# Optimization experiments

Measured on AMD Instinct MI355X. Metric: run time of the kernel, lower is better.

The kernel has to match this reference:

```python
import jax, jax.numpy as jnp
import numpy as np

N_NODES = 100000
N_EDGES = 300000
N_TYPES = 3
HID = 128
EMB = 64
N_GRAPHS = 4096
T_STEPS = 4


def setup_inputs() -> dict:
    key = jax.random.key(0)
    ks = jax.random.split(key, 12)
    s = 1.0 / np.sqrt(HID)
    return {
        "node_features": jax.random.normal(ks[0], (N_NODES, HID), jnp.float32),
        "edge_index": jax.random.randint(ks[1], (N_TYPES, 2, N_EDGES), 0, N_NODES),
        "node_to_graph_id": jnp.sort(jax.random.randint(ks[2], (N_NODES,), 0, N_GRAPHS)),
        "W_msg": jax.random.normal(ks[3], (N_TYPES, HID, HID), jnp.float32) * s,
        "b_msg": jnp.zeros((N_TYPES, HID), jnp.float32),
        "W_ih": jax.random.normal(ks[4], (3 * HID, HID), jnp.float32) * s,
        "W_hh": jax.random.normal(ks[5], (3 * HID, HID), jnp.float32) * s,
        "b_ih": jnp.zeros((3 * HID,), jnp.float32),
        "b_hh": jnp.zeros((3 * HID,), jnp.float32),
        "W_proj": jax.random.normal(ks[6], (EMB, HID), jnp.float32) * s,
        "b_proj": jnp.zeros((EMB,), jnp.float32),
        "W_gate": jax.random.normal(ks[7], (EMB, HID), jnp.float32) * s,
        "b_gate": jnp.zeros((EMB,), jnp.float32),
    }


def _gru_cell(m, h, W_ih, W_hh, b_ih, b_hh):
    # torch.nn.GRUCell math; gates ordered (r, z, n)
    gi = m @ W_ih.T + b_ih          # [N, 3H]
    gh = h @ W_hh.T + b_hh          # [N, 3H]
    i_r, i_z, i_n = jnp.split(gi, 3, axis=-1)
    h_r, h_z, h_n = jnp.split(gh, 3, axis=-1)
    r = jax.nn.sigmoid(i_r + h_r)
    z = jax.nn.sigmoid(i_z + h_z)
    n = jnp.tanh(i_n + r * h_n)
    return (1.0 - z) * n + z * h


def reference(node_features, edge_index, node_to_graph_id,
              W_msg, b_msg, W_ih, W_hh, b_ih, b_hh,
              W_proj, b_proj, W_gate, b_gate):
    h = node_features  # [N, H]

    def per_type(eidx, W, b, h):
        src, dst = eidx[0], eidx[1]
        m = h[src] @ W + b  # gather + per-edge-type linear, [E, H]
        return jax.ops.segment_sum(m, dst, num_segments=N_NODES)

    for _ in range(T_STEPS):  # fixed small T: python loop is fine
        msgs = jax.vmap(per_type, in_axes=(0, 0, 0, None))(edge_index, W_msg, b_msg, h)
        m = msgs.sum(axis=0)  # [N, H] aggregated over edge types
        h = _gru_cell(m, h, W_ih, W_hh, b_ih, b_hh)

    # gated index_add graph readout (mlp_down is identity)
    proj = h @ W_proj.T + b_proj                 # [N, E]
    gate = jax.nn.sigmoid(h @ W_gate.T + b_gate)  # [N, E]
    graph_feats = jax.ops.segment_sum(gate * proj, node_to_graph_id,
                                      num_segments=N_GRAPHS)
    return graph_feats
```

## Files before the change

kernel.cpp:

```cpp
#include <hip/hip_runtime.h>
#include <hip/hip_bf16.h>
#include <math.h>

#define NN 100000
#define NNP 100096
#define NE 300000
#define HID 128
#define EMB 64
#define NG 4096
#define DEG_CAP 32
#define XS 512

typedef __bf16 bf16x8 __attribute__((ext_vector_type(8)));
typedef float  f32x16 __attribute__((ext_vector_type(16)));
typedef short  short8 __attribute__((ext_vector_type(8)));

typedef const __attribute__((address_space(1))) unsigned int* gas_u32;
typedef __attribute__((address_space(3))) unsigned int* las_u32;

__device__ __forceinline__ void gload16(const void* g, void* l) {
    __builtin_amdgcn_global_load_lds((gas_u32)g, (las_u32)l, 16, 0, 0);
}
__device__ __forceinline__ void gload16nt(const void* g, void* l) {
    __builtin_amdgcn_global_load_lds((gas_u32)g, (las_u32)l, 16, 0, 2);
}

__device__ __forceinline__ float bf2f(unsigned short u) {
    unsigned int x = ((unsigned int)u) << 16;
    return __builtin_bit_cast(float, x);
}
__device__ __forceinline__ unsigned short f2bf(float f) {
    unsigned int x = __builtin_bit_cast(unsigned int, f);
    unsigned int r = x + 0x7fff + ((x >> 16) & 1);
    return (unsigned short)(r >> 16);
}
__device__ __forceinline__ float sigm(float x) { return 1.f / (1.f + __expf(-x)); }

__global__ __launch_bounds__(256) void k_init(const float* __restrict__ nf,
                                              unsigned short* __restrict__ Y) {
    int id = blockIdx.x * 256 + threadIdx.x;
    int n = id >> 7, c = id & 127;
    Y[(long)n * HID + c] = (n < NN) ? f2bf(nf[(long)n * HID + c]) : (unsigned short)0;
}

__global__ __launch_bounds__(256) void k_build_csr(const int* __restrict__ ei,
                                                   int* __restrict__ deg,
                                                   int* __restrict__ csr) {
    int id = blockIdx.x * 256 + threadIdx.x;
    if (id >= 3 * NE) return;
    int t = id / NE;
    int i = id - t * NE;
    int src = ei[(t * 2 + 0) * NE + i];
    int dst = ei[(t * 2 + 1) * NE + i];
    int p = atomicAdd(&deg[t * NN + dst], 1);
    if (p < DEG_CAP) csr[((long)t * NN + dst) * DEG_CAP + p] = src;
}

__global__ __launch_bounds__(256) void k_pack_deg(const int* __restrict__ deg,
                                                  int4* __restrict__ degp) {
    int n = blockIdx.x * 256 + threadIdx.x;
    if (n >= NNP) return;
    int4 v; v.x = 0; v.y = 0; v.z = 0; v.w = 0;
    if (n < NN) { v.x = deg[n]; v.y = deg[NN + n]; v.z = deg[2 * NN + n]; }
    degp[n] = v;
}

__global__ __launch_bounds__(512) void k_build_w(const float* __restrict__ Wmsg,
                                                 const float* __restrict__ Wih,
                                                 const float* __restrict__ Whh,
                                                 unsigned short* __restrict__ Bf) {
    int np = blockIdx.x;
    int k = threadIdx.x;
    int c = np >> 2, sec = np & 3;
    float v = 0.f;
    if (k < 384) {
        if (sec < 3) {
            int t = k >> 7, kk = k & 127;
            const float* wm = Wmsg + ((long)t * HID + kk) * HID;
            const float* wi = Wih + (long)(sec * HID + c) * HID;
            float s = 0.f;
            for (int j = 0; j < HID; j++) s += wm[j] * wi[j];
            v = s;
        }
    } else {
        int kk = k - 384;
        if (sec == 0)      v = Whh[(long)c * HID + kk];
        else if (sec == 1) v = Whh[(long)(HID + c) * HID + kk];
        else if (sec == 3) v = Whh[(long)(2 * HID + c) * HID + kk];
    }
    int nb = np >> 5, nl = np & 31;
    int k16 = k >> 4, kgg = (k >> 3) & 1, e = k & 7;
    Bf[((((nb * 32 + k16) * 2 + kgg) * 32 + nl) << 3) + e] = f2bf(v);
}

__global__ __launch_bounds__(512) void k_build_bias(const float* __restrict__ bih,
                                                    const float* __restrict__ bhh,
                                                    const float* __restrict__ bmsg,
                                                    const float* __restrict__ Wih,
                                                    float* __restrict__ bbig,
                                                    float* __restrict__ Bdeg) {
    int np = threadIdx.x;
    int c = np >> 2, sec = np & 3;
    float b;
    if (sec == 0)      b = bih[c] + bhh[c];
    else if (sec == 1) b = bih[HID + c] + bhh[HID + c];
    else if (sec == 2) b = bih[2 * HID + c];
    else               b = bhh[2 * HID + c];
    bbig[np] = b;
    for (int t = 0; t < 3; t++) {
        float s = 0.f;
        if (sec < 3) {
            const float* wi = Wih + (long)(sec * HID + c) * HID;
            const float* bm = bmsg + t * HID;
            for (int j = 0; j < HID; j++) s += bm[j] * wi[j];
        }
        Bdeg[t * 512 + np] = s;
    }
}

__global__ __launch_bounds__(256) void k_agg(const unsigned short* __restrict__ Y,
                                             unsigned short* __restrict__ X,
                                             const int* __restrict__ deg,
                                             const int* __restrict__ csr) {
    const int lane = threadIdx.x & 63;
    const long n = (long)blockIdx.x * 4 + (threadIdx.x >> 6);
    const int g = lane >> 4;
    const int c16 = lane & 15;
    const int l31 = lane & 31;

    int d[3], il[3];
#pragma unroll
    for (int t = 0; t < 3; t++) {
        int dt = deg[t * NN + n];
        d[t] = dt > DEG_CAP ? DEG_CAP : dt;
        il[t] = csr[((long)t * NN + n) * DEG_CAP + l31];
    }
#pragma unroll
    for (int t = 0; t < 3; t++) {
        float acc[8] = {0.f, 0.f, 0.f, 0.f, 0.f, 0.f, 0.f, 0.f};
        int rounds = (d[t] + 3) >> 2;
        for (int r = 0; r < rounds; r++) {
            int j = r * 4 + g;
            int idx = __shfl(il[t], j & 31);
            if (j < d[t]) {
                short8 v = *(const short8*)(Y + (long)idx * HID + c16 * 8);
#pragma unroll
                for (int q = 0; q < 8; q++) acc[q] += bf2f((unsigned short)v[q]);
            }
        }
#pragma unroll
        for (int q = 0; q < 8; q++) {
            acc[q] += __shfl_xor(acc[q], 16);
            acc[q] += __shfl_xor(acc[q], 32);
        }
        if (g == 0) {
            short8 o;
#pragma unroll
            for (int q = 0; q < 8; q++) o[q] = (short)f2bf(acc[q]);
            *(short8*)(X + n * XS + t * HID + c16 * 8) = o;
        }
    }
    if (g == 1) {
        short8 v = *(const short8*)(Y + n * HID + c16 * 8);
        *(short8*)(X + n * XS + 384 + c16 * 8) = v;
    }
}

__global__ __launch_bounds__(512, 4) void k_gru_mfma(
        const unsigned short* __restrict__ X,
        const unsigned short* __restrict__ Y,
        unsigned short* __restrict__ Yw,
        const unsigned short* __restrict__ Bf,
        const float* __restrict__ bbig, const float* __restrict__ Bdeg,
        const int4* __restrict__ degp) {
    __shared__ char lds[65536];

    const int tid = threadIdx.x;
    const int lane = tid & 63;
    const int wv = tid >> 6;
    const int r31 = lane & 31;
    const int kg = lane >> 5;
    const int bnN = blockIdx.x;
    const long row0 = (long)blockIdx.y * 64;

    f32x16 acc0 = (f32x16)(0.0f);
    f32x16 acc1 = (f32x16)(0.0f);

    {
        const char* base = (const char*)X + (row0 + r31) * 1024 + kg * 16;
#pragma unroll
        for (int jj = 0; jj < 8; jj++) {
            const int f = wv * 8 + jj;
            gload16nt(base + (f & 1) * 32768 + (f >> 1) * 32, lds + f * 1024);
        }
    }

    const unsigned short* pB = Bf + (long)(bnN * 8 + wv) * 16384 + lane * 8;

    short8 bs0 = *(const short8*)(pB);
    short8 bs1 = *(const short8*)(pB + 512);
    short8 bs2 = *(const short8*)(pB + 1024);
    short8 bs3 = *(const short8*)(pB + 1536);

    __syncthreads();

#pragma unroll
    for (int it = 0; it < 32; it++) {
        short8 a0 = *(const short8*)(lds + (it * 2 + 0) * 1024 + lane * 16);
        short8 a1 = *(const short8*)(lds + (it * 2 + 1) * 1024 + lane * 16);
        short8 b;
        if ((it & 3) == 0) b = bs0;
        else if ((it & 3) == 1) b = bs1;
        else if ((it & 3) == 2) b = bs2;
        else b = bs3;
        if (it + 4 < 32) {
            const short8 nb = *(const short8*)(pB + (it + 4) * 512);
            if ((it & 3) == 0) bs0 = nb;
            else if ((it & 3) == 1) bs1 = nb;
            else if ((it & 3) == 2) bs2 = nb;
            else bs3 = nb;
        }
        acc0 = __builtin_amdgcn_mfma_f32_32x32x16_bf16(
            __builtin_bit_cast(bf16x8, a0), __builtin_bit_cast(bf16x8, b), acc0, 0, 0, 0);
        acc1 = __builtin_amdgcn_mfma_f32_32x32x16_bf16(
            __builtin_bit_cast(bf16x8, a1), __builtin_bit_cast(bf16x8, b), acc1, 0, 0, 0);
    }

    float* EX = (float*)lds;
    const int ch = lane;
    const int gch = bnN * 64 + ch;
    const float4 bb = *(const float4*)(bbig + bnN * 256 + ch * 4);
    const float4 e0 = *(const float4*)(Bdeg + bnN * 256 + ch * 4);
    const float4 e1 = *(const float4*)(Bdeg + 512 + bnN * 256 + ch * 4);
    const float4 e2 = *(const float4*)(Bdeg + 1024 + bnN * 256 + ch * 4);

#pragma unroll
    for (int b = 0; b < 4; b++) {
        __syncthreads();
        {
            const int qh = (b & 1) * 8;
            const int col = wv * 32 + r31;
#pragma unroll
            for (int qq = 0; qq < 8; qq++) {
                int rwl = (qq & 3) + 8 * (qq >> 2) + 4 * kg;
                EX[rwl * 256 + col] = (b >> 1) ? acc1[qh + qq] : acc0[qh + qq];
            }
        }
        __syncthreads();
#pragma unroll
        for (int i = 0; i < 2; i++) {
            int rwl = wv + 8 * i;
            long grow = row0 + b * 16 + rwl;
            int4 dg = degp[grow];
            float dgx = (float)dg.x, dgy = (float)dg.y, dgz = (float)dg.z;
            float4 v = *(const float4*)(EX + rwl * 256 + ch * 4);
            float Sr = v.x + bb.x + dgx * e0.x + dgy * e1.x + dgz * e2.x;
            float Sz = v.y + bb.y + dgx * e0.y + dgy * e1.y + dgz * e2.y;
            float In = v.z + bb.z + dgx * e0.z + dgy * e1.z + dgz * e2.z;
            float Hn = v.w + bb.w;
            float rr = sigm(Sr);
            float zz = sigm(Sz);
            float tt = In + rr * Hn;
            float ee = __expf(2.f * tt);
            float nn = 1.f - 2.f / (ee + 1.f);
            float hv = (1.f - zz) * nn + zz * bf2f(Y[grow * HID + gch]);
            Yw[grow * HID + gch] = f2bf(hv);
        }
    }
}

__global__ __launch_bounds__(256) void k_readout(const unsigned short* __restrict__ Y,
                                                 const int* __restrict__ n2g,
                                                 const float* __restrict__ Wp,
                                                 const float* __restrict__ bp,
                                                 const float* __restrict__ Wg,
                                                 const float* __restrict__ bg,
                                                 float* __restrict__ out) {
    __shared__ float hs[32][132];
    __shared__ float Ws[64][129];
    int tid = threadIdx.x;
    long row0 = (long)blockIdx.x * 32;
    int rg = tid >> 5, cg = tid & 31;
    float acc[4][4];
#pragma unroll
    for (int r = 0; r < 4; r++)
#pragma unroll
        for (int c = 0; c < 4; c++) acc[r][c] = 0.f;

#pragma unroll
    for (int p = 0; p < 2; p++) {
        int e = p * 256 + tid;
        int r = e >> 4, c8 = e & 15;
        short8 v = *(const short8*)(Y + (row0 + r) * HID + c8 * 8);
#pragma unroll
        for (int j = 0; j < 8; j++) hs[r][c8 * 8 + j] = bf2f((unsigned short)v[j]);
    }
    for (int kc = 0; kc < 128; kc += 64) {
        __syncthreads();
#pragma unroll
        for (int p = 0; p < 8; p++) {
            int idx = p * 256 + tid;
            int j = idx >> 4, q = idx & 15;
            const float* Wsrc = (j < 64) ? Wp : Wg;
            float4 w = *(const float4*)&Wsrc[(j & 63) * HID + kc + q * 4];
            Ws[q * 4 + 0][j] = w.x;
            Ws[q * 4 + 1][j] = w.y;
            Ws[q * 4 + 2][j] = w.z;
            Ws[q * 4 + 3][j] = w.w;
        }
        __syncthreads();
#pragma unroll 8
        for (int k = 0; k < 64; k++) {
            float a[4], w[4];
#pragma unroll
            for (int r = 0; r < 4; r++) a[r] = hs[rg * 4 + r][kc + k];
#pragma unroll
            for (int c = 0; c < 4; c++) w[c] = Ws[k][cg + 32 * c];
#pragma unroll
            for (int r = 0; r < 4; r++)
#pragma unroll
                for (int c = 0; c < 4; c++) acc[r][c] += a[r] * w[c];
        }
    }
#pragma unroll
    for (int r = 0; r < 4; r++) {
        long row = row0 + rg * 4 + r;
        if (row < NN) {
            int g = n2g[row];
            float pv0 = acc[r][0] + bp[cg];
            float pv1 = acc[r][1] + bp[cg + 32];
            float gv0 = acc[r][2] + bg[cg];
            float gv1 = acc[r][3] + bg[cg + 32];
            atomicAdd(&out[g * EMB + cg],      pv0 * sigm(gv0));
            atomicAdd(&out[g * EMB + cg + 32], pv1 * sigm(gv1));
        }
    }
}

extern "C" void kernel_launch(void* const* d_in, const int* in_sizes, int n_in,
                              void* d_out, int out_size, void* d_ws, size_t ws_size,
                              hipStream_t stream) {
    const float* node_features = (const float*)d_in[0];
    const int*   edge_index    = (const int*)d_in[1];
    const int*   n2g           = (const int*)d_in[2];
    const float* W_msg         = (const float*)d_in[3];
    const float* b_msg         = (const float*)d_in[4];
    const float* W_ih          = (const float*)d_in[5];
    const float* W_hh          = (const float*)d_in[6];
    const float* b_ih          = (const float*)d_in[7];
    const float* b_hh          = (const float*)d_in[8];
    const float* W_proj        = (const float*)d_in[9];
    const float* b_proj        = (const float*)d_in[10];
    const float* W_gate        = (const float*)d_in[11];
    const float* b_gate        = (const float*)d_in[12];

    char* ws = (char*)d_ws;
    unsigned short* X    = (unsigned short*)(ws);
    unsigned short* Y    = (unsigned short*)(ws + 102498304);
    unsigned short* Bf   = (unsigned short*)(ws + 128122880);
    float*          bbig = (float*)         (ws + 128647168);
    float*          Bdeg = (float*)         (ws + 128649216);
    int4*           degp = (int4*)          (ws + 128655360);
    int*            deg  = (int*)           (ws + 130256896);
    int*            csr  = (int*)           (ws + 131456896);

    float* out = (float*)d_out;

    hipMemsetAsync(out, 0, (size_t)NG * EMB * sizeof(float), stream);
    hipMemsetAsync(deg, 0, (size_t)3 * NN * sizeof(int), stream);

    k_init<<<dim3((NNP * HID) / 256), dim3(256), 0, stream>>>(node_features, Y);
    k_build_csr<<<dim3((3 * NE + 255) / 256), dim3(256), 0, stream>>>(edge_index, deg, csr);
    k_pack_deg<<<dim3(NNP / 256), dim3(256), 0, stream>>>(deg, degp);
    k_build_w<<<dim3(512), dim3(512), 0, stream>>>(W_msg, W_ih, W_hh, Bf);
    k_build_bias<<<dim3(1), dim3(512), 0, stream>>>(b_ih, b_hh, b_msg, W_ih, bbig, Bdeg);

    for (int step = 0; step < 4; step++) {
        k_agg<<<dim3(NN / 4), dim3(256), 0, stream>>>(Y, X, deg, csr);
        k_gru_mfma<<<dim3(2, NNP / 64), dim3(512), 0, stream>>>(X, Y, Y, Bf,
                                                                bbig, Bdeg, degp);
    }
    k_readout<<<dim3(NN / 32), dim3(256), 0, stream>>>(Y, n2g, W_proj, b_proj,
                                                       W_gate, b_gate, out);
}
```

Measured before the change: 972.7 us.

## Compute full GRU output width per block with 4 waves and 2x4 MFMA tiles

The GRU MFMA kernel now gives each block all output columns for 64 rows, replacing the two column-halves that each re-loaded the same X tile. Each of the 4 waves computes 128 columns with a 2x4 grid of 32x32 accumulators, reusing each A fragment across four B fragments and prefetching B in even/odd double-buffers. The epilogue is restructured to 8 passes over 8 rows using a 512-wide LDS staging buffer, and the non-temporal load hint is dropped. This halves X traffic and LDS fills per row but raises register pressure (128 accumulator VGPRs) and lowers the thread count per block.

```diff
diff --git a/kernel.cpp b/kernel.cpp
--- a/kernel.cpp
+++ b/kernel.cpp
@@ -21,9 +21,6 @@
 __device__ __forceinline__ void gload16(const void* g, void* l) {
     __builtin_amdgcn_global_load_lds((gas_u32)g, (las_u32)l, 16, 0, 0);
 }
-__device__ __forceinline__ void gload16nt(const void* g, void* l) {
-    __builtin_amdgcn_global_load_lds((gas_u32)g, (las_u32)l, 16, 0, 2);
-}
 
 __device__ __forceinline__ float bf2f(unsigned short u) {
     unsigned int x = ((unsigned int)u) << 16;
@@ -35,6 +32,9 @@
     return (unsigned short)(r >> 16);
 }
 __device__ __forceinline__ float sigm(float x) { return 1.f / (1.f + __expf(-x)); }
+
+#define MFMA(A, B, C) __builtin_amdgcn_mfma_f32_32x32x16_bf16( \
+    __builtin_bit_cast(bf16x8, A), __builtin_bit_cast(bf16x8, B), C, 0, 0, 0)
 
 __global__ __launch_bounds__(256) void k_init(const float* __restrict__ nf,
                                               unsigned short* __restrict__ Y) {
@@ -166,7 +166,7 @@
     }
 }
 
-__global__ __launch_bounds__(512, 4) void k_gru_mfma(
+__global__ __launch_bounds__(256, 2) void k_gru_mfma(
         const unsigned short* __restrict__ X,
         const unsigned short* __restrict__ Y,
         unsigned short* __restrict__ Yw,
@@ -180,91 +180,123 @@
     const int wv = tid >> 6;
     const int r31 = lane & 31;
     const int kg = lane >> 5;
-    const int bnN = blockIdx.x;
-    const long row0 = (long)blockIdx.y * 64;
-
-    f32x16 acc0 = (f32x16)(0.0f);
-    f32x16 acc1 = (f32x16)(0.0f);
+    const long row0 = (long)blockIdx.x * 64;
+
+    f32x16 acc[2][4];
+#pragma unroll
+    for (int i = 0; i < 2; i++)
+#pragma unroll
+        for (int j = 0; j < 4; j++) acc[i][j] = (f32x16)(0.0f);
 
     {
         const char* base = (const char*)X + (row0 + r31) * 1024 + kg * 16;
 #pragma unroll
-        for (int jj = 0; jj < 8; jj++) {
-            const int f = wv * 8 + jj;
-            gload16nt(base + (f & 1) * 32768 + (f >> 1) * 32, lds + f * 1024);
-        }
-    }
-
-    const unsigned short* pB = Bf + (long)(bnN * 8 + wv) * 16384 + lane * 8;
-
-    short8 bs0 = *(const short8*)(pB);
-    short8 bs1 = *(const short8*)(pB + 512);
-    short8 bs2 = *(const short8*)(pB + 1024);
-    short8 bs3 = *(const short8*)(pB + 1536);
+        for (int jj = 0; jj < 16; jj++) {
+            const int f = wv * 16 + jj;
+            gload16(base + (f & 1) * 32768 + (f >> 1) * 32, lds + f * 1024);
+        }
+    }
+
+    const unsigned short* pB0 = Bf + (long)(wv * 4 + 0) * 16384 + lane * 8;
+    const unsigned short* pB1 = Bf + (long)(wv * 4 + 1) * 16384 + lane * 8;
+    const unsigned short* pB2 = Bf + (long)(wv * 4 + 2) * 16384 + lane * 8;
+    const unsigned short* pB3 = Bf + (long)(wv * 4 + 3) * 16384 + lane * 8;
+
+    short8 e0 = *(const short8*)(pB0);
+    short8 e1 = *(const short8*)(pB1);
+    short8 e2 = *(const short8*)(pB2);
+    short8 e3 = *(const short8*)(pB3);
+    short8 o0 = *(const short8*)(pB0 + 512);
+    short8 o1 = *(const short8*)(pB1 + 512);
+    short8 o2 = *(const short8*)(pB2 + 512);
+    short8 o3 = *(const short8*)(pB3 + 512);
 
     __syncthreads();
 
 #pragma unroll
-    for (int it = 0; it < 32; it++) {
-        short8 a0 = *(const short8*)(lds + (it * 2 + 0) * 1024 + lane * 16);
-        short8 a1 = *(const short8*)(lds + (it * 2 + 1) * 1024 + lane * 16);
-        short8 b;
-        if ((it & 3) == 0) b = bs0;
-        else if ((it & 3) == 1) b = bs1;
-        else if ((it & 3) == 2) b = bs2;
-        else b = bs3;
-        if (it + 4 < 32) {
-            const short8 nb = *(const short8*)(pB + (it + 4) * 512);
-            if ((it & 3) == 0) bs0 = nb;
-            else if ((it & 3) == 1) bs1 = nb;
-            else if ((it & 3) == 2) bs2 = nb;
-            else bs3 = nb;
-        }
-        acc0 = __builtin_amdgcn_mfma_f32_32x32x16_bf16(
-            __builtin_bit_cast(bf16x8, a0), __builtin_bit_cast(bf16x8, b), acc0, 0, 0, 0);
-        acc1 = __builtin_amdgcn_mfma_f32_32x32x16_bf16(
-            __builtin_bit_cast(bf16x8, a1), __builtin_bit_cast(bf16x8, b), acc1, 0, 0, 0);
+    for (int it = 0; it < 16; it++) {
+        const int k16 = it * 2;
+        {
+            short8 a0 = *(const short8*)(lds + (k16 * 2 + 0) * 1024 + lane * 16);
+            short8 a1 = *(const short8*)(lds + (k16 * 2 + 1) * 1024 + lane * 16);
+            acc[0][0] = MFMA(a0, e0, acc[0][0]);
+            acc[0][1] = MFMA(a0, e1, acc[0][1]);
+            acc[0][2] = MFMA(a0, e2, acc[0][2]);
+            acc[0][3] = MFMA(a0, e3, acc[0][3]);
+            acc[1][0] = MFMA(a1, e0, acc[1][0]);
+            acc[1][1] = MFMA(a1, e1, acc[1][1]);
+            acc[1][2] = MFMA(a1, e2, acc[1][2]);
+            acc[1][3] = MFMA(a1, e3, acc[1][3]);
+            if (it < 15) {
+                e0 = *(const short8*)(pB0 + (k16 + 2) * 512);
+                e1 = *(const short8*)(pB1 + (k16 + 2) * 512);
+                e2 = *(const short8*)(pB2 + (k16 + 2) * 512);
+                e3 = *(const short8*)(pB3 + (k16 + 2) * 512);
+            }
+        }
+        {
+            short8 a0 = *(const short8*)(lds + ((k16 + 1) * 2 + 0) * 1024 + lane * 16);
+            short8 a1 = *(const short8*)(lds + ((k16 + 1) * 2 + 1) * 1024 + lane * 16);
+            acc[0][0] = MFMA(a0, o0, acc[0][0]);
+            acc[0][1] = MFMA(a0, o1, acc[0][1]);
+            acc[0][2] = MFMA(a0, o2, acc[0][2]);
+            acc[0][3] = MFMA(a0, o3, acc[0][3]);
+            acc[1][0] = MFMA(a1, o0, acc[1][0]);
+            acc[1][1] = MFMA(a1, o1, acc[1][1]);
+            acc[1][2] = MFMA(a1, o2, acc[1][2]);
+            acc[1][3] = MFMA(a1, o3, acc[1][3]);
+            if (it < 15) {
+                o0 = *(const short8*)(pB0 + (k16 + 3) * 512);
+                o1 = *(const short8*)(pB1 + (k16 + 3) * 512);
+                o2 = *(const short8*)(pB2 + (k16 + 3) * 512);
+                o3 = *(const short8*)(pB3 + (k16 + 3) * 512);
+            }
+        }
     }
 
     float* EX = (float*)lds;
-    const int ch = lane;
-    const int gch = bnN * 64 + ch;
-    const float4 bb = *(const float4*)(bbig + bnN * 256 + ch * 4);
-    const float4 e0 = *(const float4*)(Bdeg + bnN * 256 + ch * 4);
-    const float4 e1 = *(const float4*)(Bdeg + 512 + bnN * 256 + ch * 4);
-    const float4 e2 = *(const float4*)(Bdeg + 1024 + bnN * 256 + ch * 4);
-
-#pragma unroll
-    for (int b = 0; b < 4; b++) {
+#pragma unroll
+    for (int b = 0; b < 8; b++) {
         __syncthreads();
         {
-            const int qh = (b & 1) * 8;
-            const int col = wv * 32 + r31;
-#pragma unroll
-            for (int qq = 0; qq < 8; qq++) {
-                int rwl = (qq & 3) + 8 * (qq >> 2) + 4 * kg;
-                EX[rwl * 256 + col] = (b >> 1) ? acc1[qh + qq] : acc0[qh + qq];
+            const int mt = b >> 2;
+            const int q1 = b & 3;
+#pragma unroll
+            for (int ct = 0; ct < 4; ct++) {
+                int col = wv * 128 + ct * 32 + r31;
+#pragma unroll
+                for (int q0 = 0; q0 < 4; q0++) {
+                    int rb = 4 * kg + q0;
+                    EX[rb * 512 + col] = acc[mt][ct][q1 * 4 + q0];
+                }
             }
         }
         __syncthreads();
-#pragma unroll
-        for (int i = 0; i < 2; i++) {
-            int rwl = wv + 8 * i;
-            long grow = row0 + b * 16 + rwl;
+        {
+            const int row = tid >> 5;
+            long grow = row0 + b * 8 + row;
             int4 dg = degp[grow];
             float dgx = (float)dg.x, dgy = (float)dg.y, dgz = (float)dg.z;
-            float4 v = *(const float4*)(EX + rwl * 256 + ch * 4);
-            float Sr = v.x + bb.x + dgx * e0.x + dgy * e1.x + dgz * e2.x;
-            float Sz = v.y + bb.y + dgx * e0.y + dgy * e1.y + dgz * e2.y;
-            float In = v.z + bb.z + dgx * e0.z + dgy * e1.z + dgz * e2.z;
-            float Hn = v.w + bb.w;
-            float rr = sigm(Sr);
-            float zz = sigm(Sz);
-            float tt = In + rr * Hn;
-            float ee = __expf(2.f * tt);
-            float nn = 1.f - 2.f / (ee + 1.f);
-            float hv = (1.f - zz) * nn + zz * bf2f(Y[grow * HID + gch]);
-            Yw[grow * HID + gch] = f2bf(hv);
+#pragma unroll
+            for (int i = 0; i < 4; i++) {
+                int ch = (tid & 31) + 32 * i;
+                float4 v  = *(const float4*)(EX + row * 512 + ch * 4);
+                float4 bb = *(const float4*)(bbig + ch * 4);
+                float4 q0 = *(const float4*)(Bdeg + ch * 4);
+                float4 q1 = *(const float4*)(Bdeg + 512 + ch * 4);
+                float4 q2 = *(const float4*)(Bdeg + 1024 + ch * 4);
+                float Sr = v.x + bb.x + dgx * q0.x + dgy * q1.x + dgz * q2.x;
+                float Sz = v.y + bb.y + dgx * q0.y + dgy * q1.y + dgz * q2.y;
+                float In = v.z + bb.z + dgx * q0.z + dgy * q1.z + dgz * q2.z;
+                float Hn = v.w + bb.w;
+                float rr = sigm(Sr);
+                float zz = sigm(Sz);
+                float tt = In + rr * Hn;
+                float ee = __expf(2.f * tt);
+                float nn = 1.f - 2.f / (ee + 1.f);
+                float hv = (1.f - zz) * nn + zz * bf2f(Y[grow * HID + ch]);
+                Yw[grow * HID + ch] = f2bf(hv);
+            }
         }
     }
 }
@@ -377,8 +409,8 @@
 
     for (int step = 0; step < 4; step++) {
         k_agg<<<dim3(NN / 4), dim3(256), 0, stream>>>(Y, X, deg, csr);
-        k_gru_mfma<<<dim3(2, NNP / 64), dim3(512), 0, stream>>>(X, Y, Y, Bf,
-                                                                bbig, Bdeg, degp);
+        k_gru_mfma<<<dim3(NNP / 64), dim3(256), 0, stream>>>(X, Y, Y, Bf,
+                                                             bbig, Bdeg, degp);
     }
     k_readout<<<dim3(NN / 32), dim3(256), 0, stream>>>(Y, n2g, W_proj, b_proj,
                                                        W_gate, b_gate, out);
```

New measurement: 970.0 us. Within noise of the previous version (-0.3%).
